# Kernel optimization log

Hardware: AMD Instinct MI355X
Metric: run time of the kernel (lower is better)

## Reference

```python
import jax, jax.numpy as jnp
import numpy as np

N_HEADS = 16
HEAD_DIM = 64
ROPE_BASE = 10000.0
EPS = 1e-6


def _rope_tables(T, hd, dtype):
    inv_freq = 1.0 / (ROPE_BASE ** (jnp.arange(0, hd, 2, dtype=jnp.float32) / hd))
    freqs = jnp.arange(T, dtype=jnp.float32)[:, None] * inv_freq[None, :]  # [T, hd/2]
    cos = jnp.cos(freqs)[None, :, None, :].astype(dtype)  # [1,T,1,hd/2]
    sin = jnp.sin(freqs)[None, :, None, :].astype(dtype)
    return cos, sin


def _apply_rope(x, cos, sin):
    d = x.shape[-1] // 2
    x1, x2 = x[..., :d], x[..., d:]
    return jnp.concatenate([x1 * cos + x2 * sin, -x1 * sin + x2 * cos], axis=-1)


def setup_inputs() -> dict:
    key = jax.random.key(0)
    k1, k2, k3, k4 = jax.random.split(key, 4)
    B, T, C = 4, 1024, 1024
    x = jax.random.normal(k1, (B, T, C), dtype=jnp.float32)
    W_qkv = jax.random.normal(k2, (3 * C, C), dtype=jnp.float32) * (1.0 / np.sqrt(C))
    W_out = jax.random.normal(k3, (C, C), dtype=jnp.float32) * (1.0 / np.sqrt(C))
    # learnable per-head curvature, init = exp(randn) * base_curvature (base=1.0)
    hyp_k = jnp.exp(jax.random.normal(k4, (1, N_HEADS, 1, 1), dtype=jnp.float32))
    return {"x": x, "W_qkv": W_qkv, "W_out": W_out, "hyp_k": hyp_k}


def reference(x, W_qkv, W_out, hyp_k):
    B, T, C = x.shape
    H, hd = N_HEADS, HEAD_DIM
    qkv = x @ W_qkv.T  # [B,T,3C]
    q, k, v = jnp.split(qkv, 3, axis=-1)
    q = q.reshape(B, T, H, hd)
    k = k.reshape(B, T, H, hd)
    v = v.reshape(B, T, H, hd)

    cos, sin = _rope_tables(T, hd, x.dtype)
    q = _apply_rope(q, cos, sin)
    k = _apply_rope(k, cos, sin)

    # [B,H,T,hd]
    q = q.transpose(0, 2, 1, 3)
    k = k.transpose(0, 2, 1, 3)
    v = v.transpose(0, 2, 1, 3)

    # Lorentz lift: x0 = sqrt(k + ||x||^2); inner = -x0*y0 + <x,y>;
    # dist = sqrt(k) * arccosh(-inner / k)  (geoopt Lorentz convention)
    kc = hyp_k[:, :, :, 0]  # [1,H,1]
    q0 = jnp.sqrt(kc + jnp.sum(q * q, axis=-1))  # [B,H,T]
    k0 = jnp.sqrt(kc + jnp.sum(k * k, axis=-1))  # [B,H,T]
    inner = jnp.einsum('bhld,bhsd->bhls', q, k) - q0[..., None] * k0[:, :, None, :]
    arg = jnp.maximum(-inner / hyp_k, 1.0 + EPS)
    dis = jnp.sqrt(hyp_k) * jnp.arccosh(arg)  # [B,H,L,S]

    attn_weight = 1.0 / (EPS + dis)
    causal = jnp.tril(jnp.ones((T, T), dtype=bool))
    attn_weight = jnp.where(causal, attn_weight, -jnp.inf)
    attn = jax.nn.softmax(attn_weight, axis=-1)
    out = jnp.einsum('bhls,bhsd->bhld', attn, v)  # [B,H,T,hd]
    out = out.transpose(0, 2, 1, 3).reshape(B, T, C)
    return out @ W_out.T
```

## Files before the change

### kernel.cpp

```cpp
#include <hip/hip_runtime.h>

#define B_ 4
#define T_ 1024
#define C_ 1024
#define H_ 16
#define HD_ 64

typedef short bf16x8 __attribute__((ext_vector_type(8)));
typedef float f32x4 __attribute__((ext_vector_type(4)));

__device__ __forceinline__ ushort f2bf(float f) {
    union { float f; unsigned u; } v; v.f = f;
    unsigned u = v.u;
    unsigned r = (u + 0x7fffu + ((u >> 16) & 1u)) >> 16;
    return (ushort)r;
}

__device__ __forceinline__ f32x4 mfma16(bf16x8 a, bf16x8 b, f32x4 c) {
    return __builtin_amdgcn_mfma_f32_16x16x32_bf16(a, b, c, 0, 0, 0);
}

__device__ __forceinline__ bf16x8 lds_frag(const ushort* base, int row, int byteoff) {
    int addr = (row * 128 + byteoff) ^ ((row & 7) << 4);
    uint4 u = *(const uint4*)((const char*)base + addr);
    return __builtin_bit_cast(bf16x8, u);
}

__device__ __forceinline__ bf16x8 lds_frag_v(const ushort* base, int d, int byteoff) {
    int addr = (d * 128 + byteoff) ^ ((((d & 7) ^ (d >> 3)) & 7) << 4);
    uint4 u = *(const uint4*)((const char*)base + addr);
    return __builtin_bit_cast(bf16x8, u);
}

__device__ __forceinline__ bf16x8 lds_frag_p(const ushort* base, int row, int byteoff) {
    int addr = (row * 128 + byteoff) ^ (((row >> 2) & 3) << 5);
    uint4 u = *(const uint4*)((const char*)base + addr);
    return __builtin_bit_cast(bf16x8, u);
}

__global__ void cast_bf16(const float* __restrict__ in, ushort* __restrict__ out, int n) {
    int i = (blockIdx.x * 256 + threadIdx.x) * 4;
    if (i >= n) return;
    float4 v = *(const float4*)(in + i);
    ushort4 o = make_ushort4(f2bf(v.x), f2bf(v.y), f2bf(v.z), f2bf(v.w));
    *(ushort4*)(out + i) = o;
}

#define GEMM_COMPUTE_128x64(As, Bs)                                                       \
    {                                                                                     \
        _Pragma("unroll")                                                                 \
        for (int ks = 0; ks < 2; ++ks) {                                                  \
            bf16x8 af[2], bfr[4];                                                         \
            _Pragma("unroll")                                                             \
            for (int mf = 0; mf < 2; ++mf)                                                \
                af[mf] = lds_frag(As, wv * 32 + mf * 16 + (lane & 15),                    \
                                  ks * 64 + ((lane >> 4) << 4));                          \
            _Pragma("unroll")                                                             \
            for (int nf = 0; nf < 4; ++nf)                                                \
                bfr[nf] = lds_frag(Bs, nf * 16 + (lane & 15),                             \
                                   ks * 64 + ((lane >> 4) << 4));                         \
            _Pragma("unroll")                                                             \
            for (int mf = 0; mf < 2; ++mf)                                                \
                _Pragma("unroll")                                                         \
                for (int nf = 0; nf < 4; ++nf)                                            \
                    acc[mf][nf] = mfma16(af[mf], bfr[nf], acc[mf][nf]);                   \
        }                                                                                 \
    }

__global__ __launch_bounds__(256) void gemm_qkv(
    const ushort* __restrict__ Xb, const ushort* __restrict__ Wb,
    const float* __restrict__ hyp,
    ushort* __restrict__ Qo, ushort* __restrict__ Ko, ushort* __restrict__ Vo,
    float* __restrict__ q0g, float* __restrict__ k0g)
{
    __shared__ ushort As[128 * 64];
    __shared__ ushort Bs[64 * 64];
    const int tid = threadIdx.x, lane = tid & 63, wv = tid >> 6;
    const int m0 = blockIdx.x * 128, n0 = blockIdx.y * 64;
    const ushort* Asrc = Xb + (size_t)m0 * C_;
    const ushort* Bsrc = Wb + (size_t)n0 * C_;

    const int srow = tid >> 3, soff = (tid & 7) * 8;
    const int swz = (srow & 7) << 4;
    uint4 a0, a1, a2, a3, b0, b1;

    auto issue = [&](int kt) {
        const ushort* Ap = Asrc + kt * 64;
        const ushort* Bp = Bsrc + kt * 64;
        a0 = *(const uint4*)(Ap + (size_t)srow * C_ + soff);
        a1 = *(const uint4*)(Ap + (size_t)(32 + srow) * C_ + soff);
        a2 = *(const uint4*)(Ap + (size_t)(64 + srow) * C_ + soff);
        a3 = *(const uint4*)(Ap + (size_t)(96 + srow) * C_ + soff);
        b0 = *(const uint4*)(Bp + (size_t)srow * C_ + soff);
        b1 = *(const uint4*)(Bp + (size_t)(32 + srow) * C_ + soff);
    };
    auto lwrite = [&]() {
        *(uint4*)((char*)As + ((tid * 16) ^ swz)) = a0;
        *(uint4*)((char*)As + (((tid + 256) * 16) ^ swz)) = a1;
        *(uint4*)((char*)As + (((tid + 512) * 16) ^ swz)) = a2;
        *(uint4*)((char*)As + (((tid + 768) * 16) ^ swz)) = a3;
        *(uint4*)((char*)Bs + ((tid * 16) ^ swz)) = b0;
        *(uint4*)((char*)Bs + (((tid + 256) * 16) ^ swz)) = b1;
    };

    issue(0);

    f32x4 acc[2][4] = {};
    for (int kt = 0; kt < 16; ++kt) {
        __syncthreads();
        lwrite();
        if (kt + 1 < 16) issue(kt + 1);
        __syncthreads();
        GEMM_COMPUTE_128x64(As, Bs);
    }

    const int sector = n0 >> 10;
    const int h = (n0 & 1023) >> 6;
    const float kc = hyp[h];
    const float inv_k = 1.0f / kc;
    float invf[2];
    invf[0] = __expf(-0.28782313662425572f * (float)(lane & 15));
    invf[1] = __expf(-0.28782313662425572f * (float)(16 + (lane & 15)));

#pragma unroll
    for (int mf = 0; mf < 2; ++mf) {
        float o[4][4];
#pragma unroll
        for (int nf = 0; nf < 4; ++nf)
#pragma unroll
            for (int r = 0; r < 4; ++r) o[nf][r] = acc[mf][nf][r];

        if (sector < 2) {
#pragma unroll
            for (int p = 0; p < 2; ++p) {
#pragma unroll
                for (int r = 0; r < 4; ++r) {
                    int m = m0 + wv * 32 + mf * 16 + ((lane >> 4) << 2) + r;
                    int t = m & (T_ - 1);
                    float sn, cs; __sincosf((float)t * invf[p], &sn, &cs);
                    float x1 = o[p][r], x2 = o[p + 2][r];
                    o[p][r]     =  x1 * cs + x2 * sn;
                    o[p + 2][r] = -x1 * sn + x2 * cs;
                }
            }
        }

#pragma unroll
        for (int r = 0; r < 4; ++r) {
            int m = m0 + wv * 32 + mf * 16 + ((lane >> 4) << 2) + r;
            int b = m >> 10, t = m & (T_ - 1);
            int bh = b * H_ + h;
            size_t base = ((size_t)bh * T_ + t) * HD_;
            float nrm = 0.f;
#pragma unroll
            for (int nf = 0; nf < 4; ++nf) {
                int d = nf * 16 + (lane & 15);
                float v = o[nf][r];
                nrm += v * v;
                ushort bv = f2bf(sector == 1 ? v * inv_k : v);
                if (sector == 0)      Qo[base + d] = bv;
                else if (sector == 1) Ko[base + d] = bv;
                else                  Vo[base + d] = bv;
            }
            if (sector < 2) {
#pragma unroll
                for (int mk = 1; mk < 16; mk <<= 1) nrm += __shfl_xor(nrm, mk);
                if ((lane & 15) == 0) {
                    float v0 = sqrtf(kc + nrm);
                    if (sector == 0) q0g[(size_t)bh * T_ + t] = v0;
                    else             k0g[(size_t)bh * T_ + t] = v0 * inv_k;
                }
            }
        }
    }
}

__global__ __launch_bounds__(256, 2) void attn_fwd(
    const ushort* __restrict__ Q, const ushort* __restrict__ K, const ushort* __restrict__ V,
    const float* __restrict__ q0g, const float* __restrict__ k0g,
    const float* __restrict__ hyp, ushort* __restrict__ AO)
{
    __shared__ ushort Ks[64 * 64];
    __shared__ ushort Vts[64 * 64];
    __shared__ ushort Ps[8][16 * 64];
    __shared__ float k0s[64];

    const int tid = threadIdx.x, lane = tid & 63, wv = tid >> 6;
    const int pr = blockIdx.x >> 6;
    const int bh = blockIdx.x & 63;
    const int h = bh & (H_ - 1);
    const int qa = pr, qb = 15 - pr, nt = qb + 1;
    const float c3 = sqrtf(hyp[h]) * 0.48045301391820142f;
    const float e3 = 6.931471805599453e-07f;

    const ushort* Kb = K + (size_t)bh * T_ * HD_;
    const ushort* Vb = V + (size_t)bh * T_ * HD_;

    bf16x8 aqA[2], aqB[2];
    {
        const ushort* qA = Q + ((size_t)bh * T_ + qa * 64 + wv * 16 + (lane & 15)) * HD_;
        const ushort* qB = Q + ((size_t)bh * T_ + qb * 64 + wv * 16 + (lane & 15)) * HD_;
#pragma unroll
        for (int ks = 0; ks < 2; ++ks) {
            aqA[ks] = __builtin_bit_cast(bf16x8, *(const uint4*)(qA + ks * 32 + ((lane >> 4) << 3)));
            aqB[ks] = __builtin_bit_cast(bf16x8, *(const uint4*)(qB + ks * 32 + ((lane >> 4) << 3)));
        }
    }
    float q0A[4], q0B[4];
#pragma unroll
    for (int r = 0; r < 4; ++r) {
        int rr = wv * 16 + ((lane >> 4) << 2) + r;
        q0A[r] = q0g[(size_t)bh * T_ + qa * 64 + rr];
        q0B[r] = q0g[(size_t)bh * T_ + qb * 64 + rr];
    }

    f32x4 oaccA[4] = {}, oaccB[4] = {};
    float lpA[4] = {}, lpB[4] = {};

    const int krow = tid >> 3, koff = tid & 7;
    const int sp = tid >> 3, dc = tid & 7;
    uint4 kv0, kv1, vv0, vv1;
    float kz = 0.f;
    auto issue = [&](int s0) {
        kv0 = *(const uint4*)(Kb + (size_t)(s0 + krow) * HD_ + koff * 8);
        kv1 = *(const uint4*)(Kb + (size_t)(s0 + 32 + krow) * HD_ + koff * 8);
        vv0 = *(const uint4*)(Vb + (size_t)(s0 + 2 * sp) * HD_ + dc * 8);
        vv1 = *(const uint4*)(Vb + (size_t)(s0 + 2 * sp + 1) * HD_ + dc * 8);
        if (tid < 64) kz = k0g[(size_t)bh * T_ + s0 + tid];
    };

    auto geom = [&](const f32x4* sc, const float* q0, const float* k0r, float p[4][4]) {
#pragma unroll
        for (int r = 0; r < 4; ++r)
#pragma unroll
            for (int sf = 0; sf < 4; ++sf) {
                float arg = fmaf(q0[r], k0r[sf], -sc[sf][r]);
                arg = fmaxf(arg, 1.0f + 1e-6f);
                float t = fmaf(arg, arg, -1.0f);
                float u = arg + __builtin_amdgcn_sqrtf(t);
                float l2 = __builtin_amdgcn_logf(u);
                float w2 = fmaf(l2, c3, e3);
                float rv = fminf(__builtin_amdgcn_rcpf(w2), 30.0f);
                p[sf][r] = __builtin_amdgcn_exp2f(rv);
            }
    };
    auto mask_diag = [&](float p[4][4]) {
        const int qloc = wv * 16 + ((lane >> 4) << 2);
#pragma unroll
        for (int r = 0; r < 4; ++r)
#pragma unroll
            for (int sf = 0; sf < 4; ++sf)
                if (sf * 16 + (lane & 15) > qloc + r) p[sf][r] = 0.f;
    };
    auto pv_step = [&](float p[4][4], ushort* ps, const bf16x8 (&vf)[2][4],
                       f32x4* oacc, float* lp) {
#pragma unroll
        for (int r = 0; r < 4; ++r) {
            int row = ((lane >> 4) << 2) + r;
#pragma unroll
            for (int sf = 0; sf < 4; ++sf) {
                int addr = (row * 128 + (sf * 16 + (lane & 15)) * 2) ^ (((row >> 2) & 3) << 5);
                *(ushort*)((char*)ps + addr) = f2bf(p[sf][r]);
            }
            lp[r] += (p[0][r] + p[1][r]) + (p[2][r] + p[3][r]);
        }
#pragma unroll
        for (int ks = 0; ks < 2; ++ks) {
            bf16x8 ap = lds_frag_p(ps, lane & 15, ks * 64 + ((lane >> 4) << 4));
#pragma unroll
            for (int df = 0; df < 4; ++df)
                oacc[df] = mfma16(ap, vf[ks][df], oacc[df]);
        }
    };

    issue(0);

    for (int it = 0; it < nt; ++it) {
        const bool actA = (it <= qa);
        __syncthreads();
        {
            *(uint4*)((char*)Ks + ((tid * 16) ^ ((krow & 7) << 4))) = kv0;
            int c1 = tid + 256;
            *(uint4*)((char*)Ks + ((c1 * 16) ^ (((c1 >> 3) & 7) << 4))) = kv1;
            union { uint4 v; ushort u[8]; } a, b;
            a.v = vv0; b.v = vv1;
#pragma unroll
            for (int j = 0; j < 8; ++j) {
                int d = dc * 8 + j;
                uint pack = (uint)a.u[j] | ((uint)b.u[j] << 16);
                *(uint*)((char*)Vts + ((d * 128 + sp * 4) ^ (((j ^ dc) & 7) << 4))) = pack;
            }
            if (tid < 64) k0s[tid] = kz;
        }
        if (it + 1 < nt) issue((it + 1) * 64);
        __syncthreads();

        bf16x8 bk[2][4];
#pragma unroll
        for (int ks = 0; ks < 2; ++ks)
#pragma unroll
            for (int sf = 0; sf < 4; ++sf)
                bk[ks][sf] = lds_frag(Ks, sf * 16 + (lane & 15), ks * 64 + ((lane >> 4) << 4));

        float k0r[4];
#pragma unroll
        for (int sf = 0; sf < 4; ++sf) k0r[sf] = k0s[sf * 16 + (lane & 15)];

        f32x4 scB[4] = {};
#pragma unroll
        for (int ks = 0; ks < 2; ++ks)
#pragma unroll
            for (int sf = 0; sf < 4; ++sf)
                scB[sf] = mfma16(aqB[ks], bk[ks][sf], scB[sf]);
        f32x4 scA[4] = {};
        if (actA) {
#pragma unroll
            for (int ks = 0; ks < 2; ++ks)
#pragma unroll
                for (int sf = 0; sf < 4; ++sf)
                    scA[sf] = mfma16(aqA[ks], bk[ks][sf], scA[sf]);
        }

        bf16x8 vf[2][4];
#pragma unroll
        for (int ks = 0; ks < 2; ++ks)
#pragma unroll
            for (int df = 0; df < 4; ++df)
                vf[ks][df] = lds_frag_v(Vts, df * 16 + (lane & 15), ks * 64 + ((lane >> 4) << 4));

        float pB[4][4];
        geom(scB, q0B, k0r, pB);
        if (it == qb) mask_diag(pB);
        pv_step(pB, Ps[wv * 2 + 1], vf, oaccB, lpB);

        if (actA) {
            float pA[4][4];
            geom(scA, q0A, k0r, pA);
            if (it == qa) mask_diag(pA);
            pv_step(pA, Ps[wv * 2 + 0], vf, oaccA, lpA);
        }
    }

    const int b = bh >> 4;
    auto epi = [&](f32x4* oacc, float* lp, int qt) {
#pragma unroll
        for (int r = 0; r < 4; ++r) {
            float s = lp[r];
#pragma unroll
            for (int mk = 1; mk < 16; mk <<= 1) s += __shfl_xor(s, mk);
            float invl = __builtin_amdgcn_rcpf(s);
            int t = qt * 64 + wv * 16 + ((lane >> 4) << 2) + r;
            size_t base = ((size_t)b * T_ + t) * C_ + h * HD_;
#pragma unroll
            for (int df = 0; df < 4; ++df)
                AO[base + df * 16 + (lane & 15)] = f2bf(oacc[df][r] * invl);
        }
    };
    epi(oaccA, lpA, qa);
    epi(oaccB, lpB, qb);
}

__global__ __launch_bounds__(256) void gemm_out(
    const ushort* __restrict__ Ab, const ushort* __restrict__ Wb, float* __restrict__ Out)
{
    __shared__ ushort As[128 * 64];
    __shared__ ushort Bs[64 * 64];
    const int tid = threadIdx.x, lane = tid & 63, wv = tid >> 6;
    const int m0 = blockIdx.x * 128, n0 = blockIdx.y * 64;
    const ushort* Asrc = Ab + (size_t)m0 * C_;
    const ushort* Bsrc = Wb + (size_t)n0 * C_;

    const int srow = tid >> 3, soff = (tid & 7) * 8;
    const int swz = (srow & 7) << 4;
    uint4 a0, a1, a2, a3, b0, b1;

    auto issue = [&](int kt) {
        const ushort* Ap = Asrc + kt * 64;
        const ushort* Bp = Bsrc + kt * 64;
        a0 = *(const uint4*)(Ap + (size_t)srow * C_ + soff);
        a1 = *(const uint4*)(Ap + (size_t)(32 + srow) * C_ + soff);
        a2 = *(const uint4*)(Ap + (size_t)(64 + srow) * C_ + soff);
        a3 = *(const uint4*)(Ap + (size_t)(96 + srow) * C_ + soff);
        b0 = *(const uint4*)(Bp + (size_t)srow * C_ + soff);
        b1 = *(const uint4*)(Bp + (size_t)(32 + srow) * C_ + soff);
    };
    auto lwrite = [&]() {
        *(uint4*)((char*)As + ((tid * 16) ^ swz)) = a0;
        *(uint4*)((char*)As + (((tid + 256) * 16) ^ swz)) = a1;
        *(uint4*)((char*)As + (((tid + 512) * 16) ^ swz)) = a2;
        *(uint4*)((char*)As + (((tid + 768) * 16) ^ swz)) = a3;
        *(uint4*)((char*)Bs + ((tid * 16) ^ swz)) = b0;
        *(uint4*)((char*)Bs + (((tid + 256) * 16) ^ swz)) = b1;
    };

    issue(0);

    f32x4 acc[2][4] = {};
    for (int kt = 0; kt < 16; ++kt) {
        __syncthreads();
        lwrite();
        if (kt + 1 < 16) issue(kt + 1);
        __syncthreads();
        GEMM_COMPUTE_128x64(As, Bs);
    }

#pragma unroll
    for (int mf = 0; mf < 2; ++mf)
#pragma unroll
        for (int r = 0; r < 4; ++r) {
            int m = m0 + wv * 32 + mf * 16 + ((lane >> 4) << 2) + r;
#pragma unroll
            for (int nf = 0; nf < 4; ++nf) {
                int n = n0 + nf * 16 + (lane & 15);
                Out[(size_t)m * C_ + n] = acc[mf][nf][r];
            }
        }
}

extern "C" void kernel_launch(void* const* d_in, const int* in_sizes, int n_in,
                              void* d_out, int out_size, void* d_ws, size_t ws_size,
                              hipStream_t stream)
{
    const float* x    = (const float*)d_in[0];
    const float* wqkv = (const float*)d_in[1];
    const float* wout = (const float*)d_in[2];
    const float* hyp  = (const float*)d_in[3];

    char* ws = (char*)d_ws;
    ushort* xb    = (ushort*)(ws + 0);
    ushort* wqkvb = (ushort*)(ws + 8388608);
    ushort* woutb = (ushort*)(ws + 14680064);
    ushort* Qb    = (ushort*)(ws + 16777216);
    ushort* Kb    = (ushort*)(ws + 25165824);
    ushort* Vb    = (ushort*)(ws + 33554432);
    ushort* Ab    = (ushort*)(ws + 41943040);
    float*  q0    = (float*)(ws + 50331648);
    float*  k0    = (float*)(ws + 50593792);

    cast_bf16<<<4096, 256, 0, stream>>>(x, xb, 4194304);
    cast_bf16<<<3072, 256, 0, stream>>>(wqkv, wqkvb, 3145728);
    cast_bf16<<<1024, 256, 0, stream>>>(wout, woutb, 1048576);

    gemm_qkv<<<dim3(32, 48), 256, 0, stream>>>(xb, wqkvb, hyp, Qb, Kb, Vb, q0, k0);
    attn_fwd<<<512, 256, 0, stream>>>(Qb, Kb, Vb, q0, k0, hyp, Ab);
    gemm_out<<<dim3(32, 16), 256, 0, stream>>>(Ab, woutb, (float*)d_out);
}
```

Baseline: 102.7 us.

## Load GEMM A fragments directly from global, fuse casts, shrink attention P buffer

Both GEMMs stop staging the A tile through shared memory and instead load MFMA A fragments straight from global memory into registers, prefetched one k-tile ahead, so only B goes through LDS. The three bf16 cast launches are merged into one kernel to cut launch overhead. The attention kernel reuses one P staging buffer per wave for both query tiles, halving its LDS footprint. Direct A loads are less coalesced and rely on cache hits, and sharing the P buffer depends on in-order use within each wave.

```diff
diff --git a/kernel.cpp b/kernel.cpp
--- a/kernel.cpp
+++ b/kernel.cpp
@@ -38,34 +38,20 @@
     return __builtin_bit_cast(bf16x8, u);
 }
 
-__global__ void cast_bf16(const float* __restrict__ in, ushort* __restrict__ out, int n) {
+__global__ void cast_all(const float* __restrict__ x, const float* __restrict__ wqkv,
+                         const float* __restrict__ wout,
+                         ushort* __restrict__ xb, ushort* __restrict__ wqkvb,
+                         ushort* __restrict__ woutb) {
     int i = (blockIdx.x * 256 + threadIdx.x) * 4;
-    if (i >= n) return;
-    float4 v = *(const float4*)(in + i);
+    const float* src; ushort* dst; int off;
+    if (i < 4194304)      { src = x;    dst = xb;    off = i; }
+    else if (i < 7340032) { src = wqkv; dst = wqkvb; off = i - 4194304; }
+    else                  { src = wout; dst = woutb; off = i - 7340032; }
+    float4 v = *(const float4*)(src + off);
     ushort4 o = make_ushort4(f2bf(v.x), f2bf(v.y), f2bf(v.z), f2bf(v.w));
-    *(ushort4*)(out + i) = o;
-}
-
-#define GEMM_COMPUTE_128x64(As, Bs)                                                       \
-    {                                                                                     \
-        _Pragma("unroll")                                                                 \
-        for (int ks = 0; ks < 2; ++ks) {                                                  \
-            bf16x8 af[2], bfr[4];                                                         \
-            _Pragma("unroll")                                                             \
-            for (int mf = 0; mf < 2; ++mf)                                                \
-                af[mf] = lds_frag(As, wv * 32 + mf * 16 + (lane & 15),                    \
-                                  ks * 64 + ((lane >> 4) << 4));                          \
-            _Pragma("unroll")                                                             \
-            for (int nf = 0; nf < 4; ++nf)                                                \
-                bfr[nf] = lds_frag(Bs, nf * 16 + (lane & 15),                             \
-                                   ks * 64 + ((lane >> 4) << 4));                         \
-            _Pragma("unroll")                                                             \
-            for (int mf = 0; mf < 2; ++mf)                                                \
-                _Pragma("unroll")                                                         \
-                for (int nf = 0; nf < 4; ++nf)                                            \
-                    acc[mf][nf] = mfma16(af[mf], bfr[nf], acc[mf][nf]);                   \
-        }                                                                                 \
-    }
+    *(ushort4*)(dst + off) = o;
+}
+
 
 __global__ __launch_bounds__(256) void gemm_qkv(
     const ushort* __restrict__ Xb, const ushort* __restrict__ Wb,
@@ -73,45 +59,56 @@
     ushort* __restrict__ Qo, ushort* __restrict__ Ko, ushort* __restrict__ Vo,
     float* __restrict__ q0g, float* __restrict__ k0g)
 {
-    __shared__ ushort As[128 * 64];
     __shared__ ushort Bs[64 * 64];
     const int tid = threadIdx.x, lane = tid & 63, wv = tid >> 6;
     const int m0 = blockIdx.x * 128, n0 = blockIdx.y * 64;
-    const ushort* Asrc = Xb + (size_t)m0 * C_;
     const ushort* Bsrc = Wb + (size_t)n0 * C_;
+    const ushort* Arow = Xb + (size_t)(m0 + wv * 32 + (lane & 15)) * C_ + ((lane >> 4) << 3);
 
     const int srow = tid >> 3, soff = (tid & 7) * 8;
     const int swz = (srow & 7) << 4;
-    uint4 a0, a1, a2, a3, b0, b1;
-
-    auto issue = [&](int kt) {
-        const ushort* Ap = Asrc + kt * 64;
+    uint4 b0, b1;
+    auto issueB = [&](int kt) {
         const ushort* Bp = Bsrc + kt * 64;
-        a0 = *(const uint4*)(Ap + (size_t)srow * C_ + soff);
-        a1 = *(const uint4*)(Ap + (size_t)(32 + srow) * C_ + soff);
-        a2 = *(const uint4*)(Ap + (size_t)(64 + srow) * C_ + soff);
-        a3 = *(const uint4*)(Ap + (size_t)(96 + srow) * C_ + soff);
         b0 = *(const uint4*)(Bp + (size_t)srow * C_ + soff);
         b1 = *(const uint4*)(Bp + (size_t)(32 + srow) * C_ + soff);
     };
-    auto lwrite = [&]() {
-        *(uint4*)((char*)As + ((tid * 16) ^ swz)) = a0;
-        *(uint4*)((char*)As + (((tid + 256) * 16) ^ swz)) = a1;
-        *(uint4*)((char*)As + (((tid + 512) * 16) ^ swz)) = a2;
-        *(uint4*)((char*)As + (((tid + 768) * 16) ^ swz)) = a3;
+    auto lwriteB = [&]() {
         *(uint4*)((char*)Bs + ((tid * 16) ^ swz)) = b0;
         *(uint4*)((char*)Bs + (((tid + 256) * 16) ^ swz)) = b1;
     };
-
-    issue(0);
+    auto lda = [&](int kt, int mf, int ks) {
+        return __builtin_bit_cast(bf16x8,
+            *(const uint4*)(Arow + (size_t)mf * 16 * C_ + kt * 64 + ks * 32));
+    };
+
+    issueB(0);
+    bf16x8 x00 = lda(0, 0, 0), x01 = lda(0, 0, 1), x10 = lda(0, 1, 0), x11 = lda(0, 1, 1);
 
     f32x4 acc[2][4] = {};
     for (int kt = 0; kt < 16; ++kt) {
         __syncthreads();
-        lwrite();
-        if (kt + 1 < 16) issue(kt + 1);
-        __syncthreads();
-        GEMM_COMPUTE_128x64(As, Bs);
+        lwriteB();
+        if (kt + 1 < 16) issueB(kt + 1);
+        __syncthreads();
+        const int ktn = (kt + 1 < 16) ? kt + 1 : kt;
+        bf16x8 y00 = lda(ktn, 0, 0), y01 = lda(ktn, 0, 1);
+        bf16x8 y10 = lda(ktn, 1, 0), y11 = lda(ktn, 1, 1);
+#pragma unroll
+        for (int ks = 0; ks < 2; ++ks) {
+            bf16x8 bfr[4];
+#pragma unroll
+            for (int nf = 0; nf < 4; ++nf)
+                bfr[nf] = lds_frag(Bs, nf * 16 + (lane & 15), ks * 64 + ((lane >> 4) << 4));
+            bf16x8 a0f = ks ? x01 : x00;
+            bf16x8 a1f = ks ? x11 : x10;
+#pragma unroll
+            for (int nf = 0; nf < 4; ++nf) {
+                acc[0][nf] = mfma16(a0f, bfr[nf], acc[0][nf]);
+                acc[1][nf] = mfma16(a1f, bfr[nf], acc[1][nf]);
+            }
+        }
+        x00 = y00; x01 = y01; x10 = y10; x11 = y11;
     }
 
     const int sector = n0 >> 10;
@@ -182,7 +179,7 @@
 {
     __shared__ ushort Ks[64 * 64];
     __shared__ ushort Vts[64 * 64];
-    __shared__ ushort Ps[8][16 * 64];
+    __shared__ ushort Ps[4][16 * 64];
     __shared__ float k0s[64];
 
     const int tid = threadIdx.x, lane = tid & 63, wv = tid >> 6;
@@ -331,13 +328,13 @@
         float pB[4][4];
         geom(scB, q0B, k0r, pB);
         if (it == qb) mask_diag(pB);
-        pv_step(pB, Ps[wv * 2 + 1], vf, oaccB, lpB);
+        pv_step(pB, Ps[wv], vf, oaccB, lpB);
 
         if (actA) {
             float pA[4][4];
             geom(scA, q0A, k0r, pA);
             if (it == qa) mask_diag(pA);
-            pv_step(pA, Ps[wv * 2 + 0], vf, oaccA, lpA);
+            pv_step(pA, Ps[wv], vf, oaccA, lpA);
         }
     }
 
@@ -363,45 +360,56 @@
 __global__ __launch_bounds__(256) void gemm_out(
     const ushort* __restrict__ Ab, const ushort* __restrict__ Wb, float* __restrict__ Out)
 {
-    __shared__ ushort As[128 * 64];
     __shared__ ushort Bs[64 * 64];
     const int tid = threadIdx.x, lane = tid & 63, wv = tid >> 6;
     const int m0 = blockIdx.x * 128, n0 = blockIdx.y * 64;
-    const ushort* Asrc = Ab + (size_t)m0 * C_;
     const ushort* Bsrc = Wb + (size_t)n0 * C_;
+    const ushort* Arow = Ab + (size_t)(m0 + wv * 32 + (lane & 15)) * C_ + ((lane >> 4) << 3);
 
     const int srow = tid >> 3, soff = (tid & 7) * 8;
     const int swz = (srow & 7) << 4;
-    uint4 a0, a1, a2, a3, b0, b1;
-
-    auto issue = [&](int kt) {
-        const ushort* Ap = Asrc + kt * 64;
+    uint4 b0, b1;
+    auto issueB = [&](int kt) {
         const ushort* Bp = Bsrc + kt * 64;
-        a0 = *(const uint4*)(Ap + (size_t)srow * C_ + soff);
-        a1 = *(const uint4*)(Ap + (size_t)(32 + srow) * C_ + soff);
-        a2 = *(const uint4*)(Ap + (size_t)(64 + srow) * C_ + soff);
-        a3 = *(const uint4*)(Ap + (size_t)(96 + srow) * C_ + soff);
         b0 = *(const uint4*)(Bp + (size_t)srow * C_ + soff);
         b1 = *(const uint4*)(Bp + (size_t)(32 + srow) * C_ + soff);
     };
-    auto lwrite = [&]() {
-        *(uint4*)((char*)As + ((tid * 16) ^ swz)) = a0;
-        *(uint4*)((char*)As + (((tid + 256) * 16) ^ swz)) = a1;
-        *(uint4*)((char*)As + (((tid + 512) * 16) ^ swz)) = a2;
-        *(uint4*)((char*)As + (((tid + 768) * 16) ^ swz)) = a3;
+    auto lwriteB = [&]() {
         *(uint4*)((char*)Bs + ((tid * 16) ^ swz)) = b0;
         *(uint4*)((char*)Bs + (((tid + 256) * 16) ^ swz)) = b1;
     };
-
-    issue(0);
+    auto lda = [&](int kt, int mf, int ks) {
+        return __builtin_bit_cast(bf16x8,
+            *(const uint4*)(Arow + (size_t)mf * 16 * C_ + kt * 64 + ks * 32));
+    };
+
+    issueB(0);
+    bf16x8 x00 = lda(0, 0, 0), x01 = lda(0, 0, 1), x10 = lda(0, 1, 0), x11 = lda(0, 1, 1);
 
     f32x4 acc[2][4] = {};
     for (int kt = 0; kt < 16; ++kt) {
         __syncthreads();
-        lwrite();
-        if (kt + 1 < 16) issue(kt + 1);
-        __syncthreads();
-        GEMM_COMPUTE_128x64(As, Bs);
+        lwriteB();
+        if (kt + 1 < 16) issueB(kt + 1);
+        __syncthreads();
+        const int ktn = (kt + 1 < 16) ? kt + 1 : kt;
+        bf16x8 y00 = lda(ktn, 0, 0), y01 = lda(ktn, 0, 1);
+        bf16x8 y10 = lda(ktn, 1, 0), y11 = lda(ktn, 1, 1);
+#pragma unroll
+        for (int ks = 0; ks < 2; ++ks) {
+            bf16x8 bfr[4];
+#pragma unroll
+            for (int nf = 0; nf < 4; ++nf)
+                bfr[nf] = lds_frag(Bs, nf * 16 + (lane & 15), ks * 64 + ((lane >> 4) << 4));
+            bf16x8 a0f = ks ? x01 : x00;
+            bf16x8 a1f = ks ? x11 : x10;
+#pragma unroll
+            for (int nf = 0; nf < 4; ++nf) {
+                acc[0][nf] = mfma16(a0f, bfr[nf], acc[0][nf]);
+                acc[1][nf] = mfma16(a1f, bfr[nf], acc[1][nf]);
+            }
+        }
+        x00 = y00; x01 = y01; x10 = y10; x11 = y11;
     }
 
 #pragma unroll
@@ -437,9 +445,7 @@
     float*  q0    = (float*)(ws + 50331648);
     float*  k0    = (float*)(ws + 50593792);
 
-    cast_bf16<<<4096, 256, 0, stream>>>(x, xb, 4194304);
-    cast_bf16<<<3072, 256, 0, stream>>>(wqkv, wqkvb, 3145728);
-    cast_bf16<<<1024, 256, 0, stream>>>(wout, woutb, 1048576);
+    cast_all<<<8192, 256, 0, stream>>>(x, wqkv, wout, xb, wqkvb, woutb);
 
     gemm_qkv<<<dim3(32, 48), 256, 0, stream>>>(xb, wqkvb, hyp, Qb, Kb, Vb, q0, k0);
     attn_fwd<<<512, 256, 0, stream>>>(Qb, Kb, Vb, q0, k0, hyp, Ab);
```

Measured after the change: 118.8 us. 15.6% more time.
